# Performance work log

Measured on AMD Instinct MI355X. Metric: run time of the kernel, lower is better.

The kernel has to match this reference:

```python
import jax, jax.numpy as jnp
import numpy as np

HIDDEN = 2048
NUM_HEADS = 32
NUM_KV_HEADS = 8
GROUP = NUM_HEADS // NUM_KV_HEADS  # 4
HEAD_DIM = HIDDEN // NUM_HEADS     # 64
SEQ = 2048


def setup_inputs() -> dict:
    key = jax.random.key(0)
    ks = jax.random.split(key, 5)
    s = HIDDEN ** -0.5
    x = jax.random.normal(ks[0], (SEQ, HIDDEN), jnp.float32)
    q_proj = jax.random.normal(ks[1], (HIDDEN, HIDDEN), jnp.float32) * s
    k_proj = jax.random.normal(ks[2], (HIDDEN, HIDDEN // GROUP), jnp.float32) * s
    v_proj = jax.random.normal(ks[3], (HIDDEN, HIDDEN // GROUP), jnp.float32) * s
    o_proj = jax.random.normal(ks[4], (HIDDEN, HIDDEN), jnp.float32) * s
    # inv_freq = 1/rsqrt(10000**(i/d)) = sqrt(10000**(i/d)) per the original module
    inv_freq = jnp.sqrt(10000.0 ** (jnp.arange(0, HEAD_DIM, 2) / HEAD_DIM)).astype(jnp.float32)
    return {"x": x, "q_proj": q_proj, "k_proj": k_proj, "v_proj": v_proj,
            "o_proj": o_proj, "inv_freq": inv_freq}


def _rope(x, inv_freq):
    # x: [S, ..., HEAD_DIM]; rotation per the original (nonstandard) formula.
    orig_dtype = x.dtype
    x = x.astype(jnp.float32)
    seq = jnp.arange(x.shape[0])
    angles = seq[:, None] * jax.lax.stop_gradient(inv_freq)[None, :]  # [S, HEAD_DIM//2]
    bshape = (x.shape[0],) + (1,) * (x.ndim - 2) + (HEAD_DIM // 2,)
    sins = jnp.sin(angles).reshape(bshape)
    coss = jnp.cos(angles).reshape(bshape)
    half, odd = jnp.split(x, 2, axis=-1)
    out = jnp.concatenate([half * coss + odd * sins, half * sins - odd * coss], axis=-1)
    return out.astype(orig_dtype)


def reference(x, q_proj, k_proj, v_proj, o_proj, inv_freq):
    S = x.shape[0]
    q = (x @ q_proj).reshape(S, NUM_KV_HEADS, GROUP, HEAD_DIM)
    k = (x @ k_proj).reshape(S, NUM_KV_HEADS, HEAD_DIM)
    v = (x @ v_proj).reshape(S, NUM_KV_HEADS, HEAD_DIM)
    q = _rope(q, inv_freq)
    k = _rope(k, inv_freq)
    # scores: [a=S, b=S, h=kv_heads, g=group]
    scores = jnp.einsum('ahgd,bhd->abhg', q, k) / (HEAD_DIM ** 0.5)
    mask = jnp.tril(jnp.ones((S, S), dtype=jnp.bool_))[:, :, None, None]
    scores = jnp.where(mask, scores, -jnp.inf)
    attn = jax.nn.softmax(scores, axis=1)  # softmax over b (axis=-3)
    o = jnp.einsum('abhg,bhd->ahgd', attn, v).reshape(S, HIDDEN)
    return o @ o_proj
```

## Files before the change

### kernel.cpp

```cpp
#include <hip/hip_runtime.h>


typedef __bf16 bf16_t;
typedef __bf16 bf16x4 __attribute__((ext_vector_type(4)));
typedef __bf16 bf16x8 __attribute__((ext_vector_type(8)));
typedef float  f32x4  __attribute__((ext_vector_type(4)));
typedef short  s16x4  __attribute__((ext_vector_type(4)));

#define S_LEN   2048
#define HID     2048
#define NKV     8
#define NH      32
#define DHEAD   64
#define KVW     (NKV * DHEAD)

__device__ __align__(16) bf16_t g_xb [S_LEN * HID];
__device__ __align__(16) bf16_t g_wTq[HID * HID];
__device__ __align__(16) bf16_t g_wTk[KVW * HID];
__device__ __align__(16) bf16_t g_wTv[KVW * HID];
__device__ __align__(16) bf16_t g_wTo[HID * HID];
__device__ __align__(16) bf16_t g_q [S_LEN * HID];
__device__ __align__(16) bf16_t g_k [S_LEN * KVW];
__device__ __align__(16) bf16_t g_vT[KVW * S_LEN];
__device__ __align__(16) bf16_t g_om[S_LEN * HID];
__device__ float g_ropeC[S_LEN * 32];
__device__ float g_ropeS[S_LEN * 32];
__device__ __align__(16) float g_po[4u * S_LEN * HID];
__device__ float g_pl[4u * S_LEN * NH];

static __device__ inline s16x4 bc4(bf16x4 v) { s16x4 r; __builtin_memcpy(&r, &v, 8); return r; }

__device__ __forceinline__ void gll16(void* lds, const void* g) {
    __builtin_amdgcn_global_load_lds(
        (const __attribute__((address_space(1))) void*)g,
        (__attribute__((address_space(3))) void*)lds,
        16, 0, 0);
}

__global__ __launch_bounds__(256)
void prep_kernel(const float* __restrict__ x,
                 const float* __restrict__ qw, const float* __restrict__ kw,
                 const float* __restrict__ vw, const float* __restrict__ ow,
                 const void* __restrict__ invf_raw) {
    __shared__ bf16_t tile[64][65];
    int b = blockIdx.x, t = threadIdx.x;

    if (b < 256) {
        int idx = b * 256 + t;
        int s = idx >> 5, j = idx & 31;
        float f;
        if (*(const unsigned*)invf_raw == 0x3F800000u) {
            f = ((const float*)invf_raw)[j];
        } else {
            unsigned u = ((unsigned)((const unsigned short*)invf_raw)[j]) << 16;
            __builtin_memcpy(&f, &u, 4);
        }
        double a = (double)s * (double)f;
        g_ropeC[idx] = (float)cos(a);
        g_ropeS[idx] = (float)sin(a);
        return;
    }
    if (b < 4352) {
        int idx = (b - 256) * 256 + t;
        float4 v = reinterpret_cast<const float4*>(x)[idx];
        bf16x4 o;
        o[0] = (bf16_t)v.x; o[1] = (bf16_t)v.y; o[2] = (bf16_t)v.z; o[3] = (bf16_t)v.w;
        *reinterpret_cast<bf16x4*>(&g_xb[(size_t)idx * 4]) = o;
        return;
    }
    const float* in; bf16_t* outp; int R, C, tb;
    if (b < 5376)      { in = qw; outp = g_wTq; R = HID; C = HID; tb = b - 4352; }
    else if (b < 5632) { in = kw; outp = g_wTk; R = HID; C = KVW; tb = b - 5376; }
    else if (b < 5888) { in = vw; outp = g_wTv; R = HID; C = KVW; tb = b - 5632; }
    else               { in = ow; outp = g_wTo; R = HID; C = HID; tb = b - 5888; }
    int xt = C >> 6;
    int c0 = (tb % xt) * 64, r0 = (tb / xt) * 64;
    int tx = t & 63, ty = t >> 6;
    #pragma unroll
    for (int r = ty; r < 64; r += 4)
        tile[r][tx] = (bf16_t)in[(size_t)(r0 + r) * C + c0 + tx];
    __syncthreads();
    #pragma unroll
    for (int r = ty; r < 64; r += 4)
        outp[(size_t)(c0 + r) * R + r0 + tx] = tile[tx][r];
}

__global__ __launch_bounds__(256)
void gemm_fused_kernel(float* __restrict__ Cf, int which) {
    __shared__ __align__(16) bf16_t As[2][64 * 64];
    __shared__ __align__(16) bf16_t Bs[2][128 * 64];

    int t    = threadIdx.x;
    int lane = t & 63, wid = t >> 6;
    int quad = lane >> 4, l15 = lane & 15;
    int bx = blockIdx.x, m0 = blockIdx.y * 64;
    int wm = (wid >> 1) * 32, wn = (wid & 1) * 64;

    const bf16_t* A; const bf16_t* Bt; int n0;
    if (which == 1)      { A = g_om; Bt = g_wTo; n0 = bx * 128; }
    else {
        A = g_xb;
        if (bx < 16)      { Bt = g_wTq; n0 = bx * 128; }
        else if (bx < 20) { Bt = g_wTk; n0 = (bx - 16) * 128; }
        else              { Bt = g_wTv; n0 = (bx - 20) * 128; }
    }

    int crow = lane >> 3;
    int gseg = (lane & 7) ^ crow;
    int so   = l15 & 7;

    f32x4 acc[2][4];
    #pragma unroll
    for (int im = 0; im < 2; ++im)
        #pragma unroll
        for (int in = 0; in < 4; ++in)
            #pragma unroll
            for (int r = 0; r < 4; ++r) acc[im][in][r] = 0.f;

    auto stage = [&](int buf, int kt) {
        int ca0 = wid * 2, cb0 = wid * 4;
        gll16(&As[buf][(ca0 + 0) * 512], A  + (size_t)(m0 + (ca0 + 0) * 8 + crow) * HID + kt + gseg * 8);
        gll16(&As[buf][(ca0 + 1) * 512], A  + (size_t)(m0 + (ca0 + 1) * 8 + crow) * HID + kt + gseg * 8);
        gll16(&Bs[buf][(cb0 + 0) * 512], Bt + (size_t)(n0 + (cb0 + 0) * 8 + crow) * HID + kt + gseg * 8);
        gll16(&Bs[buf][(cb0 + 1) * 512], Bt + (size_t)(n0 + (cb0 + 1) * 8 + crow) * HID + kt + gseg * 8);
        gll16(&Bs[buf][(cb0 + 2) * 512], Bt + (size_t)(n0 + (cb0 + 2) * 8 + crow) * HID + kt + gseg * 8);
        gll16(&Bs[buf][(cb0 + 3) * 512], Bt + (size_t)(n0 + (cb0 + 3) * 8 + crow) * HID + kt + gseg * 8);
    };

    stage(0, 0);

    for (int it = 0; it < 32; ++it) {
        int cur = it & 1;
        __syncthreads();
        if (it + 1 < 32)
            stage(cur ^ 1, (it + 1) * 64);

        bf16x8 af[2][2], bfr[4][2];
        #pragma unroll
        for (int im = 0; im < 2; ++im)
            #pragma unroll
            for (int kh = 0; kh < 2; ++kh)
                af[im][kh] = *reinterpret_cast<const bf16x8*>(
                    &As[cur][(wm + im * 16 + l15) * 64 + (((kh * 4 + quad) ^ so) * 8)]);
        #pragma unroll
        for (int in = 0; in < 4; ++in)
            #pragma unroll
            for (int kh = 0; kh < 2; ++kh)
                bfr[in][kh] = *reinterpret_cast<const bf16x8*>(
                    &Bs[cur][(wn + in * 16 + l15) * 64 + (((kh * 4 + quad) ^ so) * 8)]);
        #pragma unroll
        for (int im = 0; im < 2; ++im)
            #pragma unroll
            for (int in = 0; in < 4; ++in)
                #pragma unroll
                for (int kh = 0; kh < 2; ++kh)
                    acc[im][in] = __builtin_amdgcn_mfma_f32_16x16x32_bf16(
                        af[im][kh], bfr[in][kh], acc[im][in], 0, 0, 0);
    }

    if (which == 1) {
        #pragma unroll
        for (int im = 0; im < 2; ++im) {
            int rowb = m0 + wm + im * 16 + quad * 4;
            #pragma unroll
            for (int in = 0; in < 4; ++in) {
                int col = bx * 128 + wn + in * 16 + l15;
                #pragma unroll
                for (int r = 0; r < 4; ++r)
                    Cf[(size_t)(rowb + r) * HID + col] = acc[im][in][r];
            }
        }
    } else if (bx < 20) {
        bf16_t* Cb; int N, colbase;
        if (bx < 16) { Cb = g_q; N = HID; colbase = bx * 128 + wn; }
        else         { Cb = g_k; N = KVW; colbase = (bx - 16) * 128 + wn; }
        #pragma unroll
        for (int im = 0; im < 2; ++im) {
            #pragma unroll
            for (int r = 0; r < 4; ++r) {
                int row = m0 + wm + im * 16 + quad * 4 + r;
                #pragma unroll
                for (int in = 0; in < 2; ++in) {
                    int d = in * 16 + l15;
                    float a  = acc[im][in][r];
                    float bb = acc[im][in + 2][r];
                    float cc = g_ropeC[row * 32 + d];
                    float ss = g_ropeS[row * 32 + d];
                    Cb[(size_t)row * N + colbase + d]      = (bf16_t)(a * cc + bb * ss);
                    Cb[(size_t)row * N + colbase + 32 + d] = (bf16_t)(a * ss - bb * cc);
                }
            }
        }
    } else {
        #pragma unroll
        for (int im = 0; im < 2; ++im) {
            int rowb = m0 + wm + im * 16 + quad * 4;
            #pragma unroll
            for (int in = 0; in < 4; ++in) {
                int col = (bx - 20) * 128 + wn + in * 16 + l15;
                #pragma unroll
                for (int r = 0; r < 4; ++r)
                    g_vT[(size_t)col * S_LEN + (rowb + r)] = (bf16_t)acc[im][in][r];
            }
        }
    }
}

__global__ __launch_bounds__(256)
void flash_part_kernel() {
    __shared__ __align__(16) bf16_t Ks[64][72];
    __shared__ __align__(16) bf16_t Vs[64][72];

    int t    = threadIdx.x;
    int lane = t & 63, wid = t >> 6;
    int quad = lane >> 4, l15 = lane & 15;
    int bx   = blockIdx.x;
    int hk   = bx & 7;
    int qb32 = (bx >> 3) & 63;
    int chunk = bx >> 9;
    int nkt  = (qb32 >> 1) + 1;
    int kt0  = chunk * 8;
    if (kt0 >= nkt) return;
    int kt1  = min(kt0 + 8, nkt);

    int head = hk * 4 + wid;
    int q0   = qb32 * 32;

    bf16x8 aq[2][2];
    #pragma unroll
    for (int mq = 0; mq < 2; ++mq) {
        const bf16_t* qp = g_q + (size_t)(q0 + mq * 16 + l15) * HID + head * 64 + quad * 8;
        aq[mq][0] = *reinterpret_cast<const bf16x8*>(qp);
        aq[mq][1] = *reinterpret_cast<const bf16x8*>(qp + 32);
        #pragma unroll
        for (int j = 0; j < 8; ++j) {
            aq[mq][0][j] = (bf16_t)((float)aq[mq][0][j] * 0.125f);
            aq[mq][1][j] = (bf16_t)((float)aq[mq][1][j] * 0.125f);
        }
    }

    bf16x4 ones4;
    #pragma unroll
    for (int j = 0; j < 4; ++j) ones4[j] = (bf16_t)1.0f;
    s16x4 ones_s = bc4(ones4);

    f32x4 oacc[2][4], liacc[2];
    #pragma unroll
    for (int mq = 0; mq < 2; ++mq) {
        #pragma unroll
        for (int r = 0; r < 4; ++r) liacc[mq][r] = 0.f;
        #pragma unroll
        for (int dt = 0; dt < 4; ++dt)
            #pragma unroll
            for (int r = 0; r < 4; ++r) oacc[mq][dt][r] = 0.f;
    }

    int qcol[2] = { q0 + l15, q0 + 16 + l15 };

    for (int kt = kt0; kt < kt1; ++kt) {
        int k0 = kt * 64;
        __syncthreads();
        #pragma unroll
        for (int i = t; i < 512; i += 256) {
            int row = i >> 3, seg = i & 7;
            *reinterpret_cast<int4*>(&Ks[row][seg * 8]) =
                *reinterpret_cast<const int4*>(g_k + (size_t)(k0 + row) * KVW + hk * 64 + seg * 8);
            *reinterpret_cast<int4*>(&Vs[row][seg * 8]) =
                *reinterpret_cast<const int4*>(g_vT + (size_t)(hk * 64 + row) * S_LEN + k0 + seg * 8);
        }
        __syncthreads();

        bf16x8 ak[4][2];
        #pragma unroll
        for (int mk = 0; mk < 4; ++mk) {
            ak[mk][0] = *reinterpret_cast<const bf16x8*>(&Ks[mk * 16 + l15][quad * 8]);
            ak[mk][1] = *reinterpret_cast<const bf16x8*>(&Ks[mk * 16 + l15][32 + quad * 8]);
        }

        f32x4 sacc[4][2];
        #pragma unroll
        for (int mk = 0; mk < 4; ++mk)
            #pragma unroll
            for (int mq = 0; mq < 2; ++mq) {
                f32x4 s;
                #pragma unroll
                for (int r = 0; r < 4; ++r) s[r] = 0.f;
                s = __builtin_amdgcn_mfma_f32_16x16x32_bf16(ak[mk][0], aq[mq][0], s, 0, 0, 0);
                s = __builtin_amdgcn_mfma_f32_16x16x32_bf16(ak[mk][1], aq[mq][1], s, 0, 0, 0);
                sacc[mk][mq] = s;
            }

        s16x4 pas[4][2];
        #pragma unroll
        for (int mk = 0; mk < 4; ++mk)
            #pragma unroll
            for (int mq = 0; mq < 2; ++mq) {
                bf16x4 pa;
                #pragma unroll
                for (int r = 0; r < 4; ++r) {
                    int kk = k0 + mk * 16 + quad * 4 + r;
                    pa[r] = (bf16_t)((kk <= qcol[mq]) ? __expf(sacc[mk][mq][r] - 16.0f) : 0.0f);
                }
                pas[mk][mq] = bc4(pa);
            }

        #pragma unroll
        for (int mk = 0; mk < 4; ++mk) {
            #pragma unroll
            for (int dt = 0; dt < 4; ++dt) {
                bf16x4 bv = *reinterpret_cast<const bf16x4*>(&Vs[dt * 16 + l15][mk * 16 + quad * 4]);
                s16x4 bvs = bc4(bv);
                #pragma unroll
                for (int mq = 0; mq < 2; ++mq)
                    oacc[mq][dt] = __builtin_amdgcn_mfma_f32_16x16x16bf16_1k(pas[mk][mq], bvs, oacc[mq][dt], 0, 0, 0);
            }
            #pragma unroll
            for (int mq = 0; mq < 2; ++mq)
                liacc[mq] = __builtin_amdgcn_mfma_f32_16x16x16bf16_1k(pas[mk][mq], ones_s, liacc[mq], 0, 0, 0);
        }
    }

    float* po = g_po + (size_t)chunk * S_LEN * HID;
    #pragma unroll
    for (int mq = 0; mq < 2; ++mq)
        #pragma unroll
        for (int r = 0; r < 4; ++r) {
            int row = q0 + mq * 16 + quad * 4 + r;
            #pragma unroll
            for (int dt = 0; dt < 4; ++dt)
                po[(size_t)row * HID + head * 64 + dt * 16 + l15] = oacc[mq][dt][r];
            if (l15 == 0)
                g_pl[((size_t)chunk * S_LEN + row) * NH + head] = liacc[mq][r];
        }
}

__global__ __launch_bounds__(256)
void flash_combine_kernel() {
    int t = blockIdx.x * 256 + threadIdx.x;
    int row  = t >> 9;
    int col4 = (t & 511) * 4;
    int head = col4 >> 6;
    int nkt  = ((row >> 5) >> 1) + 1;
    int nc   = (nkt + 7) >> 3;

    float4 s = make_float4(0.f, 0.f, 0.f, 0.f);
    float l = 0.f;
    for (int c = 0; c < nc; ++c) {
        const float4 v = *reinterpret_cast<const float4*>(
            g_po + ((size_t)c * S_LEN + row) * HID + col4);
        s.x += v.x; s.y += v.y; s.z += v.z; s.w += v.w;
        l += g_pl[((size_t)c * S_LEN + row) * NH + head];
    }
    float inv = 1.0f / l;
    bf16x4 o;
    o[0] = (bf16_t)(s.x * inv); o[1] = (bf16_t)(s.y * inv);
    o[2] = (bf16_t)(s.z * inv); o[3] = (bf16_t)(s.w * inv);
    *reinterpret_cast<bf16x4*>(&g_om[(size_t)row * HID + col4]) = o;
}

extern "C" void kernel_launch(void* const* d_in, const int* in_sizes, int n_in,
                              void* d_out, int out_size, void* d_ws, size_t ws_size,
                              hipStream_t stream) {
    const float* x    = (const float*)d_in[0];
    const float* qpW  = (const float*)d_in[1];
    const float* kpW  = (const float*)d_in[2];
    const float* vpW  = (const float*)d_in[3];
    const float* opW  = (const float*)d_in[4];
    const void*  invf = d_in[5];
    float* out = (float*)d_out;

    prep_kernel<<<6912, 256, 0, stream>>>(x, qpW, kpW, vpW, opW, invf);
    gemm_fused_kernel<<<dim3(24, 32), 256, 0, stream>>>(nullptr, 0);
    flash_part_kernel<<<2048, 256, 0, stream>>>();
    flash_combine_kernel<<<4096, 256, 0, stream>>>();
    gemm_fused_kernel<<<dim3(16, 32), 256, 0, stream>>>(out, 1);
}
```

Baseline: 251.6 us.

## Load GEMM B operand directly from global into registers, bypassing LDS

```diff
diff --git a/kernel.cpp b/kernel.cpp
--- a/kernel.cpp
+++ b/kernel.cpp
@@ -88,7 +88,6 @@
 __global__ __launch_bounds__(256)
 void gemm_fused_kernel(float* __restrict__ Cf, int which) {
     __shared__ __align__(16) bf16_t As[2][64 * 64];
-    __shared__ __align__(16) bf16_t Bs[2][128 * 64];
 
     int t    = threadIdx.x;
     int lane = t & 63, wid = t >> 6;
@@ -108,6 +107,7 @@
     int crow = lane >> 3;
     int gseg = (lane & 7) ^ crow;
     int so   = l15 & 7;
+    const bf16_t* brow = Bt + (size_t)(n0 + wn + l15) * HID + quad * 8;
 
     f32x4 acc[2][4];
     #pragma unroll
@@ -117,37 +117,25 @@
             #pragma unroll
             for (int r = 0; r < 4; ++r) acc[im][in][r] = 0.f;
 
-    auto stage = [&](int buf, int kt) {
-        int ca0 = wid * 2, cb0 = wid * 4;
-        gll16(&As[buf][(ca0 + 0) * 512], A  + (size_t)(m0 + (ca0 + 0) * 8 + crow) * HID + kt + gseg * 8);
-        gll16(&As[buf][(ca0 + 1) * 512], A  + (size_t)(m0 + (ca0 + 1) * 8 + crow) * HID + kt + gseg * 8);
-        gll16(&Bs[buf][(cb0 + 0) * 512], Bt + (size_t)(n0 + (cb0 + 0) * 8 + crow) * HID + kt + gseg * 8);
-        gll16(&Bs[buf][(cb0 + 1) * 512], Bt + (size_t)(n0 + (cb0 + 1) * 8 + crow) * HID + kt + gseg * 8);
-        gll16(&Bs[buf][(cb0 + 2) * 512], Bt + (size_t)(n0 + (cb0 + 2) * 8 + crow) * HID + kt + gseg * 8);
-        gll16(&Bs[buf][(cb0 + 3) * 512], Bt + (size_t)(n0 + (cb0 + 3) * 8 + crow) * HID + kt + gseg * 8);
+    auto stageA = [&](int buf, int kt) {
+        gll16(&As[buf][(wid * 2 + 0) * 512], A + (size_t)(m0 + (wid * 2 + 0) * 8 + crow) * HID + kt + gseg * 8);
+        gll16(&As[buf][(wid * 2 + 1) * 512], A + (size_t)(m0 + (wid * 2 + 1) * 8 + crow) * HID + kt + gseg * 8);
     };
-
-    stage(0, 0);
-
-    for (int it = 0; it < 32; ++it) {
-        int cur = it & 1;
-        __syncthreads();
-        if (it + 1 < 32)
-            stage(cur ^ 1, (it + 1) * 64);
-
-        bf16x8 af[2][2], bfr[4][2];
+    auto loadB = [&](bf16x8 (&br)[4][2], int kt) {
+        #pragma unroll
+        for (int in = 0; in < 4; ++in)
+            #pragma unroll
+            for (int kh = 0; kh < 2; ++kh)
+                br[in][kh] = *reinterpret_cast<const bf16x8*>(brow + (size_t)in * 16 * HID + kt + kh * 32);
+    };
+    auto compute = [&](const bf16_t* Abuf, bf16x8 (&br)[4][2]) {
+        bf16x8 af[2][2];
         #pragma unroll
         for (int im = 0; im < 2; ++im)
             #pragma unroll
             for (int kh = 0; kh < 2; ++kh)
                 af[im][kh] = *reinterpret_cast<const bf16x8*>(
-                    &As[cur][(wm + im * 16 + l15) * 64 + (((kh * 4 + quad) ^ so) * 8)]);
-        #pragma unroll
-        for (int in = 0; in < 4; ++in)
-            #pragma unroll
-            for (int kh = 0; kh < 2; ++kh)
-                bfr[in][kh] = *reinterpret_cast<const bf16x8*>(
-                    &Bs[cur][(wn + in * 16 + l15) * 64 + (((kh * 4 + quad) ^ so) * 8)]);
+                    &Abuf[(wm + im * 16 + l15) * 64 + (((kh * 4 + quad) ^ so) * 8)]);
         #pragma unroll
         for (int im = 0; im < 2; ++im)
             #pragma unroll
@@ -155,7 +143,20 @@
                 #pragma unroll
                 for (int kh = 0; kh < 2; ++kh)
                     acc[im][in] = __builtin_amdgcn_mfma_f32_16x16x32_bf16(
-                        af[im][kh], bfr[in][kh], acc[im][in], 0, 0, 0);
+                        af[im][kh], br[in][kh], acc[im][in], 0, 0, 0);
+    };
+
+    bf16x8 b0[4][2], b1[4][2];
+    stageA(0, 0);
+    loadB(b0, 0);
+
+    for (int it = 0; it < 32; it += 2) {
+        __syncthreads();
+        if (it + 1 < 32) { stageA(1, (it + 1) * 64); loadB(b1, (it + 1) * 64); }
+        compute(&As[0][0], b0);
+        __syncthreads();
+        if (it + 2 < 32) { stageA(0, (it + 2) * 64); loadB(b0, (it + 2) * 64); }
+        compute(&As[1][0], b1);
     }
 
     if (which == 1) {
```

Measured after the change: 341.5 us. 35.7% more time.
